# Kernel optimization log

Measured on AMD Instinct MI355X. Metric: run time of the kernel, lower is better.

The kernel has to match this reference:

```python
import jax, jax.numpy as jnp
import numpy as np


def setup_inputs() -> dict:
    key = jax.random.key(0)
    ks = jax.random.split(key, 5)
    B, S, I, H = 64, 512, 1024, 1024
    s_ih = 1.0 / np.sqrt(H)
    return {
        "x": jax.random.normal(ks[0], (B, S, I), dtype=jnp.float32),
        "W_ih": jax.random.normal(ks[1], (4 * H, I), dtype=jnp.float32) * s_ih,
        "W_hh": jax.random.normal(ks[2], (4 * H, H), dtype=jnp.float32) * s_ih,
        "b_ih": jax.random.normal(ks[3], (4 * H,), dtype=jnp.float32) * s_ih,
        "b_hh": jax.random.normal(ks[4], (4 * H,), dtype=jnp.float32) * s_ih,
    }


def _lstm_seq(x, W_ih, W_hh, b_ih, b_hh):
    B, S, _ = x.shape
    H = W_hh.shape[1]
    # Precompute input projections for all timesteps in one big GEMM: [B,S,4H]
    x_proj = jnp.einsum('bsi,gi->bsg', x, W_ih) + b_ih + b_hh

    def step(carry, xp_t):
        h, c = carry
        gates = xp_t + h @ W_hh.T  # [B,4H]
        i, f, g, o = jnp.split(gates, 4, axis=-1)  # PyTorch gate order i,f,g,o
        i = jax.nn.sigmoid(i)
        f = jax.nn.sigmoid(f)
        g = jnp.tanh(g)
        o = jax.nn.sigmoid(o)
        c = f * c + i * g
        h = o * jnp.tanh(c)
        return (h, c), h

    h0 = jnp.zeros((B, H), dtype=x.dtype)
    c0 = jnp.zeros((B, H), dtype=x.dtype)
    (h_last, c_last), h_seq = jax.lax.scan(step, (h0, c0), jnp.swapaxes(x_proj, 0, 1))
    return jnp.swapaxes(h_seq, 0, 1), h_last, c_last  # [B,S,H], [B,H], [B,H]


def reference(x, W_ih, W_hh, b_ih, b_hh):
    h_seq, h_last, c_last = _lstm_seq(x, W_ih, W_hh, b_ih, b_hh)
    return (h_seq, (h_last, c_last))
```

## Files before the change

kernel.cpp:

```cpp
#include <hip/hip_runtime.h>

#define B_ 64
#define S_ 512
#define I_ 1024
#define H_ 1024
#define G_ 4096
#define WPAD 1032
#define UREG 12

typedef __attribute__((ext_vector_type(4))) float f32x4;
typedef __attribute__((ext_vector_type(8))) short bf16x8;

static __device__ __forceinline__ ushort f2b(float f) {
    union { float f; unsigned u; } v; v.f = f;
    unsigned u = v.u;
    unsigned r = (u + 0x7fffu + ((u >> 16) & 1u)) >> 16;
    return (ushort)r;
}
static __device__ __forceinline__ float b2f(ushort b) {
    union { unsigned u; float f; } v; v.u = ((unsigned)b) << 16; return v.f;
}

__global__ __launch_bounds__(256) void conv_f2b_kernel(
    const float* __restrict__ in, ushort* __restrict__ out, int n4)
{
    int i = blockIdx.x * blockDim.x + threadIdx.x;
    int stride = gridDim.x * blockDim.x;
    for (; i < n4; i += stride) {
        float4 v = ((const float4*)in)[i];
        ushort4 o;
        o.x = f2b(v.x); o.y = f2b(v.y); o.z = f2b(v.z); o.w = f2b(v.w);
        ((ushort4*)out)[i] = o;
    }
}

__global__ __launch_bounds__(256) void xproj_mfma(
    const ushort* __restrict__ Xb, const ushort* __restrict__ Wb,
    const float* __restrict__ bih, const float* __restrict__ bhh,
    ushort* __restrict__ xp)
{
    __shared__ ushort As[128][40];
    __shared__ ushort Bs[128][40];
    const int tid  = threadIdx.x;
    const int lane = tid & 63;
    const int w    = tid >> 6;
    const int wm   = (w >> 1) * 64, wn = (w & 1) * 64;
    const int m0   = blockIdx.y * 128, n0 = blockIdx.x * 128;

    const int srow   = tid >> 2;
    const int schunk = (tid & 3) * 8;

    const ushort* Xr0 = Xb + (size_t)(m0 + srow) * I_ + schunk;
    const ushort* Xr1 = Xb + (size_t)(m0 + srow + 64) * I_ + schunk;
    const ushort* Wr0 = Wb + (size_t)(n0 + srow) * I_ + schunk;
    const ushort* Wr1 = Wb + (size_t)(n0 + srow + 64) * I_ + schunk;

    f32x4 acc[4][4];
#pragma unroll
    for (int mi = 0; mi < 4; ++mi)
#pragma unroll
        for (int ni = 0; ni < 4; ++ni)
#pragma unroll
            for (int r = 0; r < 4; ++r) acc[mi][ni][r] = 0.f;

    bf16x8 ra0 = *(const bf16x8*)Xr0;
    bf16x8 ra1 = *(const bf16x8*)Xr1;
    bf16x8 rb0 = *(const bf16x8*)Wr0;
    bf16x8 rb1 = *(const bf16x8*)Wr1;

    const int arow = lane & 15;
    const int akg  = (lane >> 4) * 8;

    for (int kt = 0; kt < 32; ++kt) {
        __syncthreads();
        *(bf16x8*)&As[srow][schunk]      = ra0;
        *(bf16x8*)&As[srow + 64][schunk] = ra1;
        *(bf16x8*)&Bs[srow][schunk]      = rb0;
        *(bf16x8*)&Bs[srow + 64][schunk] = rb1;
        __syncthreads();
        if (kt < 31) {
            int k0 = (kt + 1) * 32;
            ra0 = *(const bf16x8*)(Xr0 + k0);
            ra1 = *(const bf16x8*)(Xr1 + k0);
            rb0 = *(const bf16x8*)(Wr0 + k0);
            rb1 = *(const bf16x8*)(Wr1 + k0);
        }
        bf16x8 af[4], bfv[4];
#pragma unroll
        for (int mi = 0; mi < 4; ++mi)
            af[mi] = *(const bf16x8*)&As[wm + mi * 16 + arow][akg];
#pragma unroll
        for (int ni = 0; ni < 4; ++ni)
            bfv[ni] = *(const bf16x8*)&Bs[wn + ni * 16 + arow][akg];
#pragma unroll
        for (int mi = 0; mi < 4; ++mi)
#pragma unroll
            for (int ni = 0; ni < 4; ++ni)
                acc[mi][ni] = __builtin_amdgcn_mfma_f32_16x16x32_bf16(
                    af[mi], bfv[ni], acc[mi][ni], 0, 0, 0);
    }

    float bsum[4];
#pragma unroll
    for (int ni = 0; ni < 4; ++ni) {
        int col = n0 + wn + ni * 16 + (lane & 15);
        bsum[ni] = bih[col] + bhh[col];
    }
#pragma unroll
    for (int mi = 0; mi < 4; ++mi)
#pragma unroll
        for (int ni = 0; ni < 4; ++ni) {
            int col = n0 + wn + ni * 16 + (lane & 15);
            int g = col >> 10, hc = col & 1023;
            int cb = hc >> 4, cc = hc & 15;
#pragma unroll
            for (int r = 0; r < 4; ++r) {
                int row = m0 + wm + mi * 16 + (lane >> 4) * 4 + r;
                int bb = row >> 9, ss = row & 511;
                xp[(((size_t)ss * 64 + cb) * 64 + bb) * 64 + g * 16 + cc] =
                    f2b(acc[mi][ni][r] + bsum[ni]);
            }
        }
}

__global__ __launch_bounds__(64, 1) void lstm_persist(
    const ushort* __restrict__ Whhb, const ushort* __restrict__ xp,
    ushort* h_all, int* flags, float* __restrict__ hseq,
    float* __restrict__ hlast, float* __restrict__ clast)
{
    __shared__ ushort Ws[64 * WPAD];

    const int lane = threadIdx.x;
    const int bid  = blockIdx.x;
    const int cb   = bid >> 2;
    const int q    = bid & 3;
    const int c0   = cb * 16;
    const int l15  = lane & 15;
    const int kg   = lane >> 4;
    const int m0   = q * 16;

#pragma unroll
    for (int i = 0; i < 128; ++i) {
        int id = lane + 64 * i;
        int r  = id >> 7;
        int k8 = (id & 127) * 8;
        int g = r >> 4, cc = r & 15;
        *(bf16x8*)&Ws[r * WPAD + k8] =
            *(const bf16x8*)(Whhb + (size_t)(g * H_ + c0 + cc) * H_ + k8);
    }

    float creg[4] = {0.f, 0.f, 0.f, 0.f};
    __syncthreads();

    bf16x8 bh[UREG][4];
#pragma unroll
    for (int u = 0; u < UREG; ++u)
#pragma unroll
        for (int g = 0; g < 4; ++g)
            bh[u][g] = *(const bf16x8*)&Ws[(g * 16 + l15) * WPAD + u * 32 + kg * 8];

    ushort xu[4][4];
    {
        const ushort* xps = xp + ((size_t)0 * 64 + cb) * (64 * 64);
#pragma unroll
        for (int r = 0; r < 4; ++r)
#pragma unroll
            for (int g = 0; g < 4; ++g)
                xu[r][g] = xps[(size_t)(m0 + kg * 4 + r) * 64 + g * 16 + l15];
    }

    float hvp[4];

    for (int s = 0; s < S_; ++s) {
        const ushort* hp = h_all + (size_t)s * (B_ * H_);
        ushort*       hn = h_all + (size_t)(s + 1) * (B_ * H_);

        if (s > 0) {
            int* fp = flags + ((size_t)s * 4 + q) * 64 + lane;
            unsigned long long rdy;
            do {
                int f = __hip_atomic_load(fp, __ATOMIC_RELAXED,
                                          __HIP_MEMORY_SCOPE_AGENT);
                rdy = __ballot(f != 0);
            } while (rdy != ~0ULL);
            asm volatile("" ::: "memory");
        }

        const ushort* Ap = hp + (size_t)(m0 + l15) * H_ + kg * 8;
        bf16x8 a[32];
#pragma unroll
        for (int u = 0; u < 32; ++u) a[u] = *(const bf16x8*)(Ap + u * 32);

        if (s > 0) {
#pragma unroll
            for (int r = 0; r < 4; ++r) {
                int bb = m0 + kg * 4 + r;
                unsigned fo = __float_as_uint(hvp[r]);
                unsigned fp2 = __shfl_xor(fo, 1);
                if ((l15 & 1) == 0) {
                    unsigned long long fw = (unsigned long long)fo |
                                            ((unsigned long long)fp2 << 32);
                    *(unsigned long long*)
                        (hseq + ((size_t)bb * S_ + (s - 1)) * H_ + c0 + l15) = fw;
                }
            }
        }

        f32x4 ac0, ac1, ac2, ac3;
#pragma unroll
        for (int r = 0; r < 4; ++r) { ac0[r] = 0.f; ac1[r] = 0.f; ac2[r] = 0.f; ac3[r] = 0.f; }

#pragma unroll
        for (int u = 0; u < UREG; ++u) {
            ac0 = __builtin_amdgcn_mfma_f32_16x16x32_bf16(a[u], bh[u][0], ac0, 0, 0, 0);
            ac1 = __builtin_amdgcn_mfma_f32_16x16x32_bf16(a[u], bh[u][1], ac1, 0, 0, 0);
            ac2 = __builtin_amdgcn_mfma_f32_16x16x32_bf16(a[u], bh[u][2], ac2, 0, 0, 0);
            ac3 = __builtin_amdgcn_mfma_f32_16x16x32_bf16(a[u], bh[u][3], ac3, 0, 0, 0);
        }
#pragma unroll
        for (int u = UREG; u < 32; ++u) {
            const ushort* wp = &Ws[l15 * WPAD + u * 32 + kg * 8];
            bf16x8 b0 = *(const bf16x8*)(wp);
            bf16x8 b1 = *(const bf16x8*)(wp + 16 * WPAD);
            bf16x8 b2 = *(const bf16x8*)(wp + 32 * WPAD);
            bf16x8 b3 = *(const bf16x8*)(wp + 48 * WPAD);
            ac0 = __builtin_amdgcn_mfma_f32_16x16x32_bf16(a[u], b0, ac0, 0, 0, 0);
            ac1 = __builtin_amdgcn_mfma_f32_16x16x32_bf16(a[u], b1, ac1, 0, 0, 0);
            ac2 = __builtin_amdgcn_mfma_f32_16x16x32_bf16(a[u], b2, ac2, 0, 0, 0);
            ac3 = __builtin_amdgcn_mfma_f32_16x16x32_bf16(a[u], b3, ac3, 0, 0, 0);
        }

        float cn[4];
#pragma unroll
        for (int r = 0; r < 4; ++r) {
            float gi = ac0[r] + b2f(xu[r][0]);
            float gf = ac1[r] + b2f(xu[r][1]);
            float gg = ac2[r] + b2f(xu[r][2]);
            float go = ac3[r] + b2f(xu[r][3]);
            float ii = 1.f / (1.f + __expf(-gi));
            float ff = 1.f / (1.f + __expf(-gf));
            float gt = 1.f - 2.f / (__expf(2.f * gg) + 1.f);
            float oo = 1.f / (1.f + __expf(-go));
            cn[r] = ff * creg[r] + ii * gt;
            hvp[r] = oo * (1.f - 2.f / (__expf(2.f * cn[r]) + 1.f));
            creg[r] = cn[r];
        }

#pragma unroll
        for (int r = 0; r < 4; ++r) {
            int bb = m0 + kg * 4 + r;
            unsigned hb = (unsigned)f2b(hvp[r]);
            unsigned hpp = __shfl_xor(hb, 1);
            if ((l15 & 1) == 0) {
                unsigned hw = hb | (hpp << 16);
                __hip_atomic_store((unsigned*)(hn + (size_t)bb * H_ + c0 + l15), hw,
                                   __ATOMIC_RELAXED, __HIP_MEMORY_SCOPE_AGENT);
            }
        }
        asm volatile("s_waitcnt vmcnt(0)" ::: "memory");
        if (s < S_ - 1 && lane == 0) {
            __hip_atomic_store(flags + ((size_t)(s + 1) * 4 + q) * 64 + cb,
                               1, __ATOMIC_RELAXED, __HIP_MEMORY_SCOPE_AGENT);
        }

        if (s < S_ - 1) {
            const ushort* xps = xp + ((size_t)(s + 1) * 64 + cb) * (64 * 64);
#pragma unroll
            for (int r = 0; r < 4; ++r)
#pragma unroll
                for (int g = 0; g < 4; ++g)
                    xu[r][g] = xps[(size_t)(m0 + kg * 4 + r) * 64 + g * 16 + l15];
        } else {
#pragma unroll
            for (int r = 0; r < 4; ++r) {
                int bb = m0 + kg * 4 + r;
                unsigned fo = __float_as_uint(hvp[r]);
                unsigned fp2 = __shfl_xor(fo, 1);
                if ((l15 & 1) == 0) {
                    unsigned long long fw = (unsigned long long)fo |
                                            ((unsigned long long)fp2 << 32);
                    *(unsigned long long*)
                        (hseq + ((size_t)bb * S_ + s) * H_ + c0 + l15) = fw;
                }
                hlast[(size_t)bb * H_ + c0 + l15] = hvp[r];
                clast[(size_t)bb * H_ + c0 + l15] = cn[r];
            }
        }
    }
}

extern "C" void kernel_launch(void* const* d_in, const int* in_sizes, int n_in,
                              void* d_out, int out_size, void* d_ws, size_t ws_size,
                              hipStream_t stream) {
    const float* x   = (const float*)d_in[0];
    const float* Wih = (const float*)d_in[1];
    const float* Whh = (const float*)d_in[2];
    const float* bih = (const float*)d_in[3];
    const float* bhh = (const float*)d_in[4];
    float* out = (float*)d_out;

    ushort* xp    = (ushort*)d_ws;
    ushort* xbf   = xp + 134217728;
    ushort* wihb  = xbf + 33554432;
    ushort* whhb  = wihb + 4194304;
    ushort* h_all = whhb + 4194304;
    int*    flags = (int*)(h_all + 33619968);

    float* hseq  = out;
    float* hlast = out + (size_t)B_ * S_ * H_;
    float* clast = hlast + (size_t)B_ * H_;

    hipMemsetAsync(h_all, 0, (size_t)B_ * H_ * sizeof(ushort), stream);
    hipMemsetAsync(flags, 0, (size_t)S_ * 4 * 64 * sizeof(int), stream);

    conv_f2b_kernel<<<2048, 256, 0, stream>>>(x, xbf, (B_ * S_ * I_) / 4);
    conv_f2b_kernel<<<1024, 256, 0, stream>>>(Wih, wihb, (G_ * I_) / 4);
    conv_f2b_kernel<<<1024, 256, 0, stream>>>(Whh, whhb, (G_ * H_) / 4);

    dim3 gg(G_ / 128, (B_ * S_) / 128);
    xproj_mfma<<<gg, 256, 0, stream>>>(xbf, wihb, bih, bhh, xp);

    lstm_persist<<<256, 64, 0, stream>>>(whhb, xp, h_all, flags,
                                         hseq, hlast, clast);
}
```

Before: 3.033 ms.

## Replace flag-based step sync with sentinel-filled hidden-state polling

Drops the per-step flag array and its ballot spin-wait. The whole h_all history is prefilled with 0xFF, and each block spins on atomic loads of the h data itself until no 64-bit word equals the all-ones sentinel, so the wait and the data fetch collapse into one round trip. h stores are widened to 64-bit atomic stores so every sentinel-checked word is written in one store. The register-cached W_hh slice (UREG) is removed and all weights are read from LDS, which frees registers but adds LDS traffic. It also adds a large memset of the full h history each call.

After: 4.854 ms. +60.1%, slower.

```diff
diff --git a/kernel.cpp b/kernel.cpp
--- a/kernel.cpp
+++ b/kernel.cpp
@@ -6,7 +6,6 @@
 #define H_ 1024
 #define G_ 4096
 #define WPAD 1032
-#define UREG 12
 
 typedef __attribute__((ext_vector_type(4))) float f32x4;
 typedef __attribute__((ext_vector_type(8))) short bf16x8;
@@ -125,7 +124,7 @@
 
 __global__ __launch_bounds__(64, 1) void lstm_persist(
     const ushort* __restrict__ Whhb, const ushort* __restrict__ xp,
-    ushort* h_all, int* flags, float* __restrict__ hseq,
+    ushort* h_all, float* __restrict__ hseq,
     float* __restrict__ hlast, float* __restrict__ clast)
 {
     __shared__ ushort Ws[64 * WPAD];
@@ -152,13 +151,6 @@
     float creg[4] = {0.f, 0.f, 0.f, 0.f};
     __syncthreads();
 
-    bf16x8 bh[UREG][4];
-#pragma unroll
-    for (int u = 0; u < UREG; ++u)
-#pragma unroll
-        for (int g = 0; g < 4; ++g)
-            bh[u][g] = *(const bf16x8*)&Ws[(g * 16 + l15) * WPAD + u * 32 + kg * 8];
-
     ushort xu[4][4];
     {
         const ushort* xps = xp + ((size_t)0 * 64 + cb) * (64 * 64);
@@ -171,25 +163,30 @@
 
     float hvp[4];
 
+    union AU { unsigned long long qv[2]; bf16x8 v; };
+
     for (int s = 0; s < S_; ++s) {
         const ushort* hp = h_all + (size_t)s * (B_ * H_);
         ushort*       hn = h_all + (size_t)(s + 1) * (B_ * H_);
 
-        if (s > 0) {
-            int* fp = flags + ((size_t)s * 4 + q) * 64 + lane;
-            unsigned long long rdy;
-            do {
-                int f = __hip_atomic_load(fp, __ATOMIC_RELAXED,
-                                          __HIP_MEMORY_SCOPE_AGENT);
-                rdy = __ballot(f != 0);
-            } while (rdy != ~0ULL);
-            asm volatile("" ::: "memory");
-        }
-
         const ushort* Ap = hp + (size_t)(m0 + l15) * H_ + kg * 8;
-        bf16x8 a[32];
-#pragma unroll
-        for (int u = 0; u < 32; ++u) a[u] = *(const bf16x8*)(Ap + u * 32);
+        AU a[32];
+        while (true) {
+            bool allok = true;
+#pragma unroll
+            for (int u = 0; u < 32; ++u) {
+                unsigned long long lo = __hip_atomic_load(
+                    (const unsigned long long*)(Ap + u * 32),
+                    __ATOMIC_RELAXED, __HIP_MEMORY_SCOPE_AGENT);
+                unsigned long long hi = __hip_atomic_load(
+                    (const unsigned long long*)(Ap + u * 32 + 4),
+                    __ATOMIC_RELAXED, __HIP_MEMORY_SCOPE_AGENT);
+                a[u].qv[0] = lo;
+                a[u].qv[1] = hi;
+                allok = allok && (lo != ~0ULL) && (hi != ~0ULL);
+            }
+            if (__ballot(allok) == ~0ULL) break;
+        }
 
         if (s > 0) {
 #pragma unroll
@@ -211,23 +208,16 @@
         for (int r = 0; r < 4; ++r) { ac0[r] = 0.f; ac1[r] = 0.f; ac2[r] = 0.f; ac3[r] = 0.f; }
 
 #pragma unroll
-        for (int u = 0; u < UREG; ++u) {
-            ac0 = __builtin_amdgcn_mfma_f32_16x16x32_bf16(a[u], bh[u][0], ac0, 0, 0, 0);
-            ac1 = __builtin_amdgcn_mfma_f32_16x16x32_bf16(a[u], bh[u][1], ac1, 0, 0, 0);
-            ac2 = __builtin_amdgcn_mfma_f32_16x16x32_bf16(a[u], bh[u][2], ac2, 0, 0, 0);
-            ac3 = __builtin_amdgcn_mfma_f32_16x16x32_bf16(a[u], bh[u][3], ac3, 0, 0, 0);
-        }
-#pragma unroll
-        for (int u = UREG; u < 32; ++u) {
+        for (int u = 0; u < 32; ++u) {
             const ushort* wp = &Ws[l15 * WPAD + u * 32 + kg * 8];
             bf16x8 b0 = *(const bf16x8*)(wp);
             bf16x8 b1 = *(const bf16x8*)(wp + 16 * WPAD);
             bf16x8 b2 = *(const bf16x8*)(wp + 32 * WPAD);
             bf16x8 b3 = *(const bf16x8*)(wp + 48 * WPAD);
-            ac0 = __builtin_amdgcn_mfma_f32_16x16x32_bf16(a[u], b0, ac0, 0, 0, 0);
-            ac1 = __builtin_amdgcn_mfma_f32_16x16x32_bf16(a[u], b1, ac1, 0, 0, 0);
-            ac2 = __builtin_amdgcn_mfma_f32_16x16x32_bf16(a[u], b2, ac2, 0, 0, 0);
-            ac3 = __builtin_amdgcn_mfma_f32_16x16x32_bf16(a[u], b3, ac3, 0, 0, 0);
+            ac0 = __builtin_amdgcn_mfma_f32_16x16x32_bf16(a[u].v, b0, ac0, 0, 0, 0);
+            ac1 = __builtin_amdgcn_mfma_f32_16x16x32_bf16(a[u].v, b1, ac1, 0, 0, 0);
+            ac2 = __builtin_amdgcn_mfma_f32_16x16x32_bf16(a[u].v, b2, ac2, 0, 0, 0);
+            ac3 = __builtin_amdgcn_mfma_f32_16x16x32_bf16(a[u].v, b3, ac3, 0, 0, 0);
         }
 
         float cn[4];
@@ -250,17 +240,15 @@
         for (int r = 0; r < 4; ++r) {
             int bb = m0 + kg * 4 + r;
             unsigned hb = (unsigned)f2b(hvp[r]);
-            unsigned hpp = __shfl_xor(hb, 1);
-            if ((l15 & 1) == 0) {
-                unsigned hw = hb | (hpp << 16);
-                __hip_atomic_store((unsigned*)(hn + (size_t)bb * H_ + c0 + l15), hw,
+            unsigned w0 = hb | (__shfl_xor(hb, 1) << 16);
+            unsigned w1 = __shfl_xor(w0, 2);
+            if ((l15 & 3) == 0) {
+                unsigned long long hw = (unsigned long long)w0 |
+                                        ((unsigned long long)w1 << 32);
+                __hip_atomic_store((unsigned long long*)
+                                       (hn + (size_t)bb * H_ + c0 + l15), hw,
                                    __ATOMIC_RELAXED, __HIP_MEMORY_SCOPE_AGENT);
             }
-        }
-        asm volatile("s_waitcnt vmcnt(0)" ::: "memory");
-        if (s < S_ - 1 && lane == 0) {
-            __hip_atomic_store(flags + ((size_t)(s + 1) * 4 + q) * 64 + cb,
-                               1, __ATOMIC_RELAXED, __HIP_MEMORY_SCOPE_AGENT);
         }
 
         if (s < S_ - 1) {
@@ -304,14 +292,14 @@
     ushort* wihb  = xbf + 33554432;
     ushort* whhb  = wihb + 4194304;
     ushort* h_all = whhb + 4194304;
-    int*    flags = (int*)(h_all + 33619968);
 
     float* hseq  = out;
     float* hlast = out + (size_t)B_ * S_ * H_;
     float* clast = hlast + (size_t)B_ * H_;
 
     hipMemsetAsync(h_all, 0, (size_t)B_ * H_ * sizeof(ushort), stream);
-    hipMemsetAsync(flags, 0, (size_t)S_ * 4 * 64 * sizeof(int), stream);
+    hipMemsetAsync(h_all + (size_t)B_ * H_, 0xFF,
+                   (size_t)S_ * B_ * H_ * sizeof(ushort), stream);
 
     conv_f2b_kernel<<<2048, 256, 0, stream>>>(x, xbf, (B_ * S_ * I_) / 4);
     conv_f2b_kernel<<<1024, 256, 0, stream>>>(Wih, wihb, (G_ * I_) / 4);
@@ -320,6 +308,5 @@
     dim3 gg(G_ / 128, (B_ * S_) / 128);
     xproj_mfma<<<gg, 256, 0, stream>>>(xbf, wihb, bih, bhh, xp);
 
-    lstm_persist<<<256, 64, 0, stream>>>(whhb, xp, h_all, flags,
-                                         hseq, hlast, clast);
-}
+    lstm_persist<<<256, 64, 0, stream>>>(whhb, xp, h_all, hseq, hlast, clast);
+}
```

## Fuse fp32-to-bf16 conversion into GEMM and recurrence loads, double-buffer LDS

Applied to the files above, without the earlier changes.

Removes the three standalone fp32-to-bf16 conversion kernels. The input projection GEMM now reads fp32 x and W_ih directly and converts them in registers, and the persistent LSTM kernel does the same for W_hh while staging it into shared memory. The GEMM also gains double-buffered LDS tiles, so each k-step needs one barrier instead of two. This avoids writing and re-reading roughly 80MB of bf16 copies, at the cost of the GEMM reading twice the bytes per tile from global memory and redoing the conversion for every tile reuse.

After: 3.440 ms. 13.4% more time.

```diff
diff --git a/kernel.cpp b/kernel.cpp
--- a/kernel.cpp
+++ b/kernel.cpp
@@ -20,27 +20,22 @@
 static __device__ __forceinline__ float b2f(ushort b) {
     union { unsigned u; float f; } v; v.u = ((unsigned)b) << 16; return v.f;
 }
-
-__global__ __launch_bounds__(256) void conv_f2b_kernel(
-    const float* __restrict__ in, ushort* __restrict__ out, int n4)
-{
-    int i = blockIdx.x * blockDim.x + threadIdx.x;
-    int stride = gridDim.x * blockDim.x;
-    for (; i < n4; i += stride) {
-        float4 v = ((const float4*)in)[i];
-        ushort4 o;
-        o.x = f2b(v.x); o.y = f2b(v.y); o.z = f2b(v.z); o.w = f2b(v.w);
-        ((ushort4*)out)[i] = o;
-    }
+static __device__ __forceinline__ bf16x8 cvt8(float4 a, float4 b) {
+    bf16x8 r;
+    r[0] = (short)f2b(a.x); r[1] = (short)f2b(a.y);
+    r[2] = (short)f2b(a.z); r[3] = (short)f2b(a.w);
+    r[4] = (short)f2b(b.x); r[5] = (short)f2b(b.y);
+    r[6] = (short)f2b(b.z); r[7] = (short)f2b(b.w);
+    return r;
 }
 
 __global__ __launch_bounds__(256) void xproj_mfma(
-    const ushort* __restrict__ Xb, const ushort* __restrict__ Wb,
+    const float* __restrict__ X, const float* __restrict__ W,
     const float* __restrict__ bih, const float* __restrict__ bhh,
     ushort* __restrict__ xp)
 {
-    __shared__ ushort As[128][40];
-    __shared__ ushort Bs[128][40];
+    __shared__ ushort As[2][128][40];
+    __shared__ ushort Bs[2][128][40];
     const int tid  = threadIdx.x;
     const int lane = tid & 63;
     const int w    = tid >> 6;
@@ -50,10 +45,10 @@
     const int srow   = tid >> 2;
     const int schunk = (tid & 3) * 8;
 
-    const ushort* Xr0 = Xb + (size_t)(m0 + srow) * I_ + schunk;
-    const ushort* Xr1 = Xb + (size_t)(m0 + srow + 64) * I_ + schunk;
-    const ushort* Wr0 = Wb + (size_t)(n0 + srow) * I_ + schunk;
-    const ushort* Wr1 = Wb + (size_t)(n0 + srow + 64) * I_ + schunk;
+    const float* Xr0 = X + (size_t)(m0 + srow) * I_ + schunk;
+    const float* Xr1 = X + (size_t)(m0 + srow + 64) * I_ + schunk;
+    const float* Wr0 = W + (size_t)(n0 + srow) * I_ + schunk;
+    const float* Wr1 = W + (size_t)(n0 + srow + 64) * I_ + schunk;
 
     f32x4 acc[4][4];
 #pragma unroll
@@ -63,41 +58,48 @@
 #pragma unroll
             for (int r = 0; r < 4; ++r) acc[mi][ni][r] = 0.f;
 
-    bf16x8 ra0 = *(const bf16x8*)Xr0;
-    bf16x8 ra1 = *(const bf16x8*)Xr1;
-    bf16x8 rb0 = *(const bf16x8*)Wr0;
-    bf16x8 rb1 = *(const bf16x8*)Wr1;
+    float4 xa0 = *(const float4*)Xr0, xa1 = *(const float4*)(Xr0 + 4);
+    float4 xb0 = *(const float4*)Xr1, xb1 = *(const float4*)(Xr1 + 4);
+    float4 wa0 = *(const float4*)Wr0, wa1 = *(const float4*)(Wr0 + 4);
+    float4 wb0 = *(const float4*)Wr1, wb1 = *(const float4*)(Wr1 + 4);
+    *(bf16x8*)&As[0][srow][schunk]      = cvt8(xa0, xa1);
+    *(bf16x8*)&As[0][srow + 64][schunk] = cvt8(xb0, xb1);
+    *(bf16x8*)&Bs[0][srow][schunk]      = cvt8(wa0, wa1);
+    *(bf16x8*)&Bs[0][srow + 64][schunk] = cvt8(wb0, wb1);
+    __syncthreads();
 
     const int arow = lane & 15;
     const int akg  = (lane >> 4) * 8;
 
     for (int kt = 0; kt < 32; ++kt) {
-        __syncthreads();
-        *(bf16x8*)&As[srow][schunk]      = ra0;
-        *(bf16x8*)&As[srow + 64][schunk] = ra1;
-        *(bf16x8*)&Bs[srow][schunk]      = rb0;
-        *(bf16x8*)&Bs[srow + 64][schunk] = rb1;
-        __syncthreads();
+        const int cur = kt & 1, nxt = cur ^ 1;
         if (kt < 31) {
             int k0 = (kt + 1) * 32;
-            ra0 = *(const bf16x8*)(Xr0 + k0);
-            ra1 = *(const bf16x8*)(Xr1 + k0);
-            rb0 = *(const bf16x8*)(Wr0 + k0);
-            rb1 = *(const bf16x8*)(Wr1 + k0);
+            xa0 = *(const float4*)(Xr0 + k0); xa1 = *(const float4*)(Xr0 + k0 + 4);
+            xb0 = *(const float4*)(Xr1 + k0); xb1 = *(const float4*)(Xr1 + k0 + 4);
+            wa0 = *(const float4*)(Wr0 + k0); wa1 = *(const float4*)(Wr0 + k0 + 4);
+            wb0 = *(const float4*)(Wr1 + k0); wb1 = *(const float4*)(Wr1 + k0 + 4);
         }
         bf16x8 af[4], bfv[4];
 #pragma unroll
         for (int mi = 0; mi < 4; ++mi)
-            af[mi] = *(const bf16x8*)&As[wm + mi * 16 + arow][akg];
+            af[mi] = *(const bf16x8*)&As[cur][wm + mi * 16 + arow][akg];
 #pragma unroll
         for (int ni = 0; ni < 4; ++ni)
-            bfv[ni] = *(const bf16x8*)&Bs[wn + ni * 16 + arow][akg];
+            bfv[ni] = *(const bf16x8*)&Bs[cur][wn + ni * 16 + arow][akg];
 #pragma unroll
         for (int mi = 0; mi < 4; ++mi)
 #pragma unroll
             for (int ni = 0; ni < 4; ++ni)
                 acc[mi][ni] = __builtin_amdgcn_mfma_f32_16x16x32_bf16(
                     af[mi], bfv[ni], acc[mi][ni], 0, 0, 0);
+        if (kt < 31) {
+            *(bf16x8*)&As[nxt][srow][schunk]      = cvt8(xa0, xa1);
+            *(bf16x8*)&As[nxt][srow + 64][schunk] = cvt8(xb0, xb1);
+            *(bf16x8*)&Bs[nxt][srow][schunk]      = cvt8(wa0, wa1);
+            *(bf16x8*)&Bs[nxt][srow + 64][schunk] = cvt8(wb0, wb1);
+            __syncthreads();
+        }
     }
 
     float bsum[4];
@@ -124,7 +126,7 @@
 }
 
 __global__ __launch_bounds__(64, 1) void lstm_persist(
-    const ushort* __restrict__ Whhb, const ushort* __restrict__ xp,
+    const float* __restrict__ Whh, const ushort* __restrict__ xp,
     ushort* h_all, int* flags, float* __restrict__ hseq,
     float* __restrict__ hlast, float* __restrict__ clast)
 {
@@ -145,8 +147,10 @@
         int r  = id >> 7;
         int k8 = (id & 127) * 8;
         int g = r >> 4, cc = r & 15;
-        *(bf16x8*)&Ws[r * WPAD + k8] =
-            *(const bf16x8*)(Whhb + (size_t)(g * H_ + c0 + cc) * H_ + k8);
+        const float* src = Whh + (size_t)(g * H_ + c0 + cc) * H_ + k8;
+        float4 a0 = *(const float4*)src;
+        float4 a1 = *(const float4*)(src + 4);
+        *(bf16x8*)&Ws[r * WPAD + k8] = cvt8(a0, a1);
     }
 
     float creg[4] = {0.f, 0.f, 0.f, 0.f};
@@ -300,10 +304,7 @@
     float* out = (float*)d_out;
 
     ushort* xp    = (ushort*)d_ws;
-    ushort* xbf   = xp + 134217728;
-    ushort* wihb  = xbf + 33554432;
-    ushort* whhb  = wihb + 4194304;
-    ushort* h_all = whhb + 4194304;
+    ushort* h_all = xp + 134217728;
     int*    flags = (int*)(h_all + 33619968);
 
     float* hseq  = out;
@@ -313,13 +314,9 @@
     hipMemsetAsync(h_all, 0, (size_t)B_ * H_ * sizeof(ushort), stream);
     hipMemsetAsync(flags, 0, (size_t)S_ * 4 * 64 * sizeof(int), stream);
 
-    conv_f2b_kernel<<<2048, 256, 0, stream>>>(x, xbf, (B_ * S_ * I_) / 4);
-    conv_f2b_kernel<<<1024, 256, 0, stream>>>(Wih, wihb, (G_ * I_) / 4);
-    conv_f2b_kernel<<<1024, 256, 0, stream>>>(Whh, whhb, (G_ * H_) / 4);
-
     dim3 gg(G_ / 128, (B_ * S_) / 128);
-    xproj_mfma<<<gg, 256, 0, stream>>>(xbf, wihb, bih, bhh, xp);
-
-    lstm_persist<<<256, 64, 0, stream>>>(whhb, xp, h_all, flags,
+    xproj_mfma<<<gg, 256, 0, stream>>>(x, Wih, bih, bhh, xp);
+
+    lstm_persist<<<256, 64, 0, stream>>>(Whh, xp, h_all, flags,
                                          hseq, hlast, clast);
 }
```
